# Kernel optimization log

Measured on AMD Instinct MI355X. Metric: run time of the kernel, lower is better.

The kernel has to match this reference:

```python
import jax, jax.numpy as jnp
import numpy as np

D_MODEL = 2048
H_Q = 32
H_KV = 8
D_HEAD = D_MODEL // H_Q   # 64
G = H_Q // H_KV           # 4 query heads per kv head
B, S = 2, 2048


def setup_inputs() -> dict:
    key = jax.random.key(0)
    ks = jax.random.split(key, 7)
    s = 0.02  # weight init scale
    return {
        "q": jax.random.normal(ks[0], (B, S, D_MODEL), jnp.float32),
        "k": jax.random.normal(ks[1], (B, S, D_MODEL), jnp.float32),
        "v": jax.random.normal(ks[2], (B, S, D_MODEL), jnp.float32),
        "Wq": jax.random.normal(ks[3], (D_MODEL, D_MODEL), jnp.float32) * s,
        "Wk": jax.random.normal(ks[4], (D_MODEL, H_KV * D_HEAD), jnp.float32) * s,
        "Wv": jax.random.normal(ks[5], (D_MODEL, H_KV * D_HEAD), jnp.float32) * s,
        "Wo": jax.random.normal(ks[6], (D_MODEL, D_MODEL), jnp.float32) * s,
    }


def reference(q, k, v, Wq, Wk, Wv, Wo):
    # Projections (torch Linear with bias=False: x @ W^T; here W stored as [in,out])
    b, s, _ = q.shape
    # repeat_interleave(k, G, -2) maps kv head j -> query heads j*G..j*G+G-1,
    # i.e. query head h uses kv head h // G. Reshape q heads as (H_KV, G)
    # kv-head-major instead of materializing expanded K/V.
    qh = (q @ Wq).reshape(b, s, H_KV, G, D_HEAD)
    kh = (k @ Wk).reshape(b, s, H_KV, D_HEAD)
    vh = (v @ Wv).reshape(b, s, H_KV, D_HEAD)
    scale = 1.0 / jnp.sqrt(jnp.asarray(D_HEAD, qh.dtype))
    # scores: [B, H_KV, G, Sq, Sk]
    scores = jnp.einsum('bqhgd,bkhd->bhgqk', qh, kh) * scale
    attn = jax.nn.softmax(scores, axis=-1)
    # context: [B, Sq, H_KV, G, D_HEAD]
    ctx = jnp.einsum('bhgqk,bkhd->bqhgd', attn, vh)
    out = ctx.reshape(b, s, D_MODEL) @ Wo
    return out
```

## Files before the change

### kernel.cpp

```cpp
#include <hip/hip_runtime.h>
#include <stdint.h>


typedef __attribute__((ext_vector_type(8))) short short8;
typedef __attribute__((ext_vector_type(4))) float float4v;
typedef __attribute__((ext_vector_type(4))) unsigned short ushort4v;
typedef __attribute__((ext_vector_type(4))) unsigned int uint4v;

__device__ __forceinline__ unsigned short f2bf(float f) {
  union { float f; unsigned int u; } v; v.f = f;
  unsigned int r = v.u + 0x7fffu + ((v.u >> 16) & 1u);
  return (unsigned short)(r >> 16);
}
__device__ __forceinline__ unsigned short f2bf_trunc(float f) {
  union { float f; unsigned int u; } v; v.f = f;
  return (unsigned short)(v.u >> 16);
}
__device__ __forceinline__ unsigned int fbits(float f) {
  union { float f; unsigned int u; } v; v.f = f; return v.u;
}
__device__ __forceinline__ unsigned int pack_bf16_trunc(float lo, float hi) {
  return __builtin_amdgcn_perm(fbits(hi), fbits(lo), 0x07060302u);
}

__device__ __forceinline__ void gl2lds16(const unsigned short* g, unsigned short* l) {
  __builtin_amdgcn_global_load_lds(
      (const __attribute__((address_space(1))) void*)g,
      (__attribute__((address_space(3))) void*)l, 16, 0, 0);
}

__global__ void conv3_bf16(const float* __restrict__ q, const float* __restrict__ k,
                           const float* __restrict__ v,
                           unsigned short* __restrict__ qo, unsigned short* __restrict__ ko,
                           unsigned short* __restrict__ vo, int n4) {
  const float* in;
  unsigned short* out;
  if (blockIdx.y == 0)      { in = q; out = qo; }
  else if (blockIdx.y == 1) { in = k; out = ko; }
  else                      { in = v; out = vo; }
  for (int i = blockIdx.x * blockDim.x + threadIdx.x; i < n4; i += gridDim.x * blockDim.x) {
    const float4v a = *(const float4v*)(in + (size_t)i * 4);
    *(ushort4v*)(out + (size_t)i * 4) = (ushort4v){f2bf(a.x), f2bf(a.y), f2bf(a.z), f2bf(a.w)};
  }
}

template<bool F32IN>
__global__ void transpose_bf16(const void* __restrict__ inp, unsigned short* __restrict__ out,
                               int R, int C) {
  __shared__ unsigned short t[32][33];
  const int x0 = blockIdx.x * 32, y0 = blockIdx.y * 32;
  const int tx = threadIdx.x, ty = threadIdx.y;
#pragma unroll
  for (int i = 0; i < 4; ++i) {
    const int r = y0 + ty + i * 8, c = x0 + tx;
    if (F32IN) t[ty + i * 8][tx] = f2bf(((const float*)inp)[(size_t)r * C + c]);
    else       t[ty + i * 8][tx] = ((const unsigned short*)inp)[(size_t)r * C + c];
  }
  __syncthreads();
#pragma unroll
  for (int i = 0; i < 4; ++i)
    out[(size_t)(x0 + ty + i * 8) * R + y0 + tx] = t[tx][ty + i * 8];
}

template<int TN, bool C_BF16>
__global__ __launch_bounds__(256, 2)
void gemm_bt(const unsigned short* __restrict__ A, const unsigned short* __restrict__ Bt,
             void* __restrict__ C, int N, int K, float cscale)
{
  constexpr int NT = TN / 32;
  constexpr int BI = TN / 64;
  __shared__ unsigned short As[128][32];
  __shared__ unsigned short Bs[TN][32];

  const int tid  = threadIdx.x;
  const int wave = tid >> 6;
  const int lane = tid & 63;
  const int quad = lane >> 4;
  const int l15  = lane & 15;
  const int wm   = (wave >> 1) * 64;
  const int wn   = (wave & 1) * (TN / 2);
  const int m0   = blockIdx.y * 128;
  const int n0   = blockIdx.x * TN;

  const int srow = lane >> 2;
  const int skof = (lane & 3) * 8;

  float4v acc[4][NT];
#pragma unroll
  for (int i = 0; i < 4; ++i)
#pragma unroll
    for (int j = 0; j < NT; ++j) acc[i][j] = (float4v)0.0f;

  for (int k0 = 0; k0 < K; k0 += 32) {
    __syncthreads();
#pragma unroll
    for (int i = 0; i < 2; ++i) {
      const int row = wave * 32 + i * 16 + srow;
      gl2lds16(A + (size_t)(m0 + row) * K + k0 + skof, &As[wave * 32 + i * 16][0]);
    }
#pragma unroll
    for (int i = 0; i < BI; ++i) {
      const int row = wave * (TN / 4) + i * 16 + srow;
      gl2lds16(Bt + (size_t)(n0 + row) * K + k0 + skof, &Bs[wave * (TN / 4) + i * 16][0]);
    }
    __syncthreads();

    short8 af[4], bf[NT];
#pragma unroll
    for (int mt = 0; mt < 4; ++mt)  af[mt] = *(const short8*)&As[wm + mt * 16 + l15][quad * 8];
#pragma unroll
    for (int nt = 0; nt < NT; ++nt) bf[nt] = *(const short8*)&Bs[wn + nt * 16 + l15][quad * 8];
#pragma unroll
    for (int mt = 0; mt < 4; ++mt)
#pragma unroll
      for (int nt = 0; nt < NT; ++nt)
        acc[mt][nt] = __builtin_amdgcn_mfma_f32_16x16x32_bf16(af[mt], bf[nt], acc[mt][nt], 0, 0, 0);
  }

#pragma unroll
  for (int mt = 0; mt < 4; ++mt)
#pragma unroll
    for (int nt = 0; nt < NT; ++nt) {
      const int row = m0 + wm + mt * 16 + quad * 4;
      const int col = n0 + wn + nt * 16 + l15;
#pragma unroll
      for (int r = 0; r < 4; ++r) {
        const float val = acc[mt][nt][r] * cscale;
        if (C_BF16) ((unsigned short*)C)[(size_t)(row + r) * N + col] = f2bf(val);
        else        ((float*)C)[(size_t)(row + r) * N + col] = val;
      }
    }
}

__global__ __launch_bounds__(256, 3)
void attn_flash(const unsigned short* __restrict__ Qp,
                const unsigned short* __restrict__ Kp,
                const unsigned short* __restrict__ VpT,
                unsigned short* __restrict__ Ctx)
{
  __shared__ unsigned short Ks[2][64 * 64];
  __shared__ unsigned short VTs[2][64 * 64];

  const int tid  = threadIdx.x;
  const int wave = tid >> 6;
  const int lane = tid & 63;
  const int quad = lane >> 4;
  const int l15  = lane & 15;

  const int head = blockIdx.y;
  const int b    = head >> 5;
  const int hq   = head & 31;
  const int hkv  = hq >> 2;
  const size_t qrow = (size_t)(b * 2048 + blockIdx.x * 128 + wave * 32);

  short8 qf[2][2];
#pragma unroll
  for (int mt = 0; mt < 2; ++mt)
#pragma unroll
    for (int kc = 0; kc < 2; ++kc)
      qf[mt][kc] = *(const short8*)&Qp[(qrow + mt * 16 + l15) * 2048 + hq * 64 + kc * 32 + quad * 8];

  float4v oa[2][4];
  float4v lacc[2];
#pragma unroll
  for (int mt = 0; mt < 2; ++mt) {
    lacc[mt] = (float4v)0.0f;
#pragma unroll
    for (int dt = 0; dt < 4; ++dt) oa[mt][dt] = (float4v)0.0f;
  }
  short8 ones;
#pragma unroll
  for (int i = 0; i < 8; ++i) ones[i] = (short)0x3F80;

  auto stage = [&](int j, int bu) {
#pragma unroll
    for (int i = 0; i < 2; ++i) {
      const int s  = i * 256 + wave * 64 + lane;
      const int r  = s >> 3;
      const int lc = (s & 7) ^ (r & 7);
      const int rk = ((r >> 4) & 1) * 32 + ((r >> 2) & 3) * 8 + (r >> 5) * 4 + (r & 3);
      gl2lds16(Kp + (size_t)(b * 2048 + j * 64 + rk) * 512 + hkv * 64 + lc * 8,
               &Ks[bu][i * 2048 + wave * 512]);
      gl2lds16(VpT + (size_t)(hkv * 64 + r) * 4096 + b * 2048 + j * 64 + lc * 8,
               &VTs[bu][i * 2048 + wave * 512]);
    }
  };

  stage(0, 0);
  __syncthreads();

  for (int j = 0; j < 32; ++j) {
    const int bu = j & 1;
    if (j < 31) stage(j + 1, bu ^ 1);

    short8 kf[4][2];
#pragma unroll
    for (int nt = 0; nt < 4; ++nt) {
      const int krow = nt * 16 + l15;
      kf[nt][0] = *(const short8*)&Ks[bu][krow * 64 + ((quad ^ (l15 & 7)) * 8)];
      kf[nt][1] = *(const short8*)&Ks[bu][krow * 64 + (((4 + quad) ^ (l15 & 7)) * 8)];
    }

    __builtin_amdgcn_s_setprio(1);

    unsigned int w[2][4][2];
#pragma unroll
    for (int mt = 0; mt < 2; ++mt) {
#pragma unroll
      for (int nt = 0; nt < 4; ++nt) {
        float4v sa = (float4v)0.0f;
        sa = __builtin_amdgcn_mfma_f32_16x16x32_bf16(kf[nt][0], qf[mt][0], sa, 0, 0, 0);
        sa = __builtin_amdgcn_mfma_f32_16x16x32_bf16(kf[nt][1], qf[mt][1], sa, 0, 0, 0);
        const float e0 = __builtin_amdgcn_exp2f(sa[0]);
        const float e1 = __builtin_amdgcn_exp2f(sa[1]);
        const float e2 = __builtin_amdgcn_exp2f(sa[2]);
        const float e3 = __builtin_amdgcn_exp2f(sa[3]);
        w[mt][nt][0] = pack_bf16_trunc(e0, e1);
        w[mt][nt][1] = pack_bf16_trunc(e2, e3);
      }
    }

#pragma unroll
    for (int kc = 0; kc < 2; ++kc) {
      union { uint4v u; short8 s; } p0u, p1u;
      p0u.u = (uint4v){w[0][kc][0], w[0][kc][1], w[0][kc + 2][0], w[0][kc + 2][1]};
      p1u.u = (uint4v){w[1][kc][0], w[1][kc][1], w[1][kc + 2][0], w[1][kc + 2][1]};
      const short8 pf0 = p0u.s;
      const short8 pf1 = p1u.s;
#pragma unroll
      for (int dt = 0; dt < 4; ++dt) {
        const int vrow = dt * 16 + l15;
        const short8 vf = *(const short8*)&VTs[bu][vrow * 64 + (((kc * 4 + quad) ^ (l15 & 7)) * 8)];
        oa[0][dt] = __builtin_amdgcn_mfma_f32_16x16x32_bf16(pf0, vf, oa[0][dt], 0, 0, 0);
        oa[1][dt] = __builtin_amdgcn_mfma_f32_16x16x32_bf16(pf1, vf, oa[1][dt], 0, 0, 0);
      }
      lacc[0] = __builtin_amdgcn_mfma_f32_16x16x32_bf16(pf0, ones, lacc[0], 0, 0, 0);
      lacc[1] = __builtin_amdgcn_mfma_f32_16x16x32_bf16(pf1, ones, lacc[1], 0, 0, 0);
    }

    __builtin_amdgcn_s_setprio(0);
    __syncthreads();
  }

#pragma unroll
  for (int mt = 0; mt < 2; ++mt)
#pragma unroll
    for (int r = 0; r < 4; ++r) {
      const float inv = 1.0f / lacc[mt][r];
#pragma unroll
      for (int dt = 0; dt < 4; ++dt)
        Ctx[(qrow + mt * 16 + quad * 4 + r) * 2048 + hq * 64 + dt * 16 + l15] =
            f2bf(oa[mt][dt][r] * inv);
    }
}

extern "C" void kernel_launch(void* const* d_in, const int* in_sizes, int n_in,
                              void* d_out, int out_size, void* d_ws, size_t ws_size,
                              hipStream_t stream)
{
  const float* q  = (const float*)d_in[0];
  const float* k  = (const float*)d_in[1];
  const float* v  = (const float*)d_in[2];
  const float* Wq = (const float*)d_in[3];
  const float* Wk = (const float*)d_in[4];
  const float* Wv = (const float*)d_in[5];
  const float* Wo = (const float*)d_in[6];
  float* out = (float*)d_out;

  unsigned short* ws  = (unsigned short*)d_ws;
  unsigned short* qb  = ws;
  unsigned short* kb  = qb  + (size_t)8388608;
  unsigned short* vb  = kb  + (size_t)8388608;
  unsigned short* WT  = vb  + (size_t)8388608;
  unsigned short* Qp  = WT  + (size_t)4194304;
  unsigned short* Kp  = Qp  + (size_t)8388608;
  unsigned short* VpT = Kp  + (size_t)2097152;
  unsigned short* Ctx = qb;

  const dim3 blk(256);
  const dim3 tblk(32, 8);
  const float SM_SCALE = 0.125f * 1.44269504089f;

  conv3_bf16<<<dim3(512, 3), blk, 0, stream>>>(q, k, v, qb, kb, vb, 8388608 / 4);

  transpose_bf16<true><<<dim3(64, 64), tblk, 0, stream>>>(Wq, WT, 2048, 2048);
  gemm_bt<128, true><<<dim3(16, 32), blk, 0, stream>>>(qb, WT, Qp, 2048, 2048, SM_SCALE);

  transpose_bf16<true><<<dim3(16, 64), tblk, 0, stream>>>(Wk, WT, 2048, 512);
  gemm_bt<64, true><<<dim3(8, 32), blk, 0, stream>>>(kb, WT, Kp, 512, 2048, 1.0f);

  transpose_bf16<true><<<dim3(16, 64), tblk, 0, stream>>>(Wv, WT, 2048, 512);
  gemm_bt<64, true><<<dim3(64, 4), blk, 0, stream>>>(WT, vb, VpT, 4096, 2048, 1.0f);

  attn_flash<<<dim3(16, 64), blk, 0, stream>>>(Qp, Kp, VpT, Ctx);

  transpose_bf16<true><<<dim3(64, 64), tblk, 0, stream>>>(Wo, WT, 2048, 2048);
  gemm_bt<128, false><<<dim3(16, 32), blk, 0, stream>>>(Ctx, WT, out, 2048, 2048, 1.0f);
}
```

Measured before the change: 413.7 us.

## Merge prep kernels and K/V projections into fewer launches, raise attention occupancy

Folds the three input fp32-to-bf16 conversions and the Wq/Wk/Wv transposes into one multi-role prep launch. The K and V projection GEMMs become a single launch that dispatches on block id, and the Wo transpose moves ahead of attention. The goal is to cut kernel launch count and let small, underfilled kernels share the GPU. It also raises attn_flash launch bounds from 3 to 4 blocks per CU, which may constrain registers. The Q GEMM now writes into a workspace region that temporarily holds the transposed K/V weights, so it relies on stream ordering.

```diff
diff --git a/kernel.cpp b/kernel.cpp
--- a/kernel.cpp
+++ b/kernel.cpp
@@ -12,10 +12,6 @@
   unsigned int r = v.u + 0x7fffu + ((v.u >> 16) & 1u);
   return (unsigned short)(r >> 16);
 }
-__device__ __forceinline__ unsigned short f2bf_trunc(float f) {
-  union { float f; unsigned int u; } v; v.f = f;
-  return (unsigned short)(v.u >> 16);
-}
 __device__ __forceinline__ unsigned int fbits(float f) {
   union { float f; unsigned int u; } v; v.f = f; return v.u;
 }
@@ -29,23 +25,47 @@
       (__attribute__((address_space(3))) void*)l, 16, 0, 0);
 }
 
-__global__ void conv3_bf16(const float* __restrict__ q, const float* __restrict__ k,
-                           const float* __restrict__ v,
-                           unsigned short* __restrict__ qo, unsigned short* __restrict__ ko,
-                           unsigned short* __restrict__ vo, int n4) {
-  const float* in;
-  unsigned short* out;
-  if (blockIdx.y == 0)      { in = q; out = qo; }
-  else if (blockIdx.y == 1) { in = k; out = ko; }
-  else                      { in = v; out = vo; }
-  for (int i = blockIdx.x * blockDim.x + threadIdx.x; i < n4; i += gridDim.x * blockDim.x) {
-    const float4v a = *(const float4v*)(in + (size_t)i * 4);
-    *(ushort4v*)(out + (size_t)i * 4) = (ushort4v){f2bf(a.x), f2bf(a.y), f2bf(a.z), f2bf(a.w)};
-  }
-}
-
-template<bool F32IN>
-__global__ void transpose_bf16(const void* __restrict__ inp, unsigned short* __restrict__ out,
+__global__ void prep(const float* __restrict__ q, const float* __restrict__ k,
+                     const float* __restrict__ v,
+                     const float* __restrict__ Wq, const float* __restrict__ Wk,
+                     const float* __restrict__ Wv,
+                     unsigned short* __restrict__ qb, unsigned short* __restrict__ kb,
+                     unsigned short* __restrict__ vb,
+                     unsigned short* __restrict__ WTq, unsigned short* __restrict__ WTk,
+                     unsigned short* __restrict__ WTv)
+{
+  __shared__ unsigned short t[32][33];
+  const int z = blockIdx.z;
+  if (z >= 3) {
+    const float* in  = (z == 3) ? q : (z == 4) ? k : v;
+    unsigned short* out = (z == 3) ? qb : (z == 4) ? kb : vb;
+    const int tid = threadIdx.y * 32 + threadIdx.x;
+    const int bid = blockIdx.y * 64 + blockIdx.x;
+    for (int i = bid * 256 + tid; i < 2097152; i += 4096 * 256) {
+      const float4v a = *(const float4v*)(in + (size_t)i * 4);
+      *(ushort4v*)(out + (size_t)i * 4) = (ushort4v){f2bf(a.x), f2bf(a.y), f2bf(a.z), f2bf(a.w)};
+    }
+    return;
+  }
+  const float* in; unsigned short* out; int R, C;
+  if (z == 0)      { in = Wq; out = WTq; R = 2048; C = 2048; }
+  else if (z == 1) { in = Wk; out = WTk; R = 2048; C = 512; }
+  else             { in = Wv; out = WTv; R = 2048; C = 512; }
+  const int x0 = blockIdx.x * 32, y0 = blockIdx.y * 32;
+  if (x0 >= C) return;
+  const int tx = threadIdx.x, ty = threadIdx.y;
+#pragma unroll
+  for (int i = 0; i < 4; ++i) {
+    const int r = y0 + ty + i * 8, c = x0 + tx;
+    t[ty + i * 8][tx] = f2bf(in[(size_t)r * C + c]);
+  }
+  __syncthreads();
+#pragma unroll
+  for (int i = 0; i < 4; ++i)
+    out[(size_t)(x0 + ty + i * 8) * R + y0 + tx] = t[tx][ty + i * 8];
+}
+
+__global__ void transpose_bf16(const float* __restrict__ inp, unsigned short* __restrict__ out,
                                int R, int C) {
   __shared__ unsigned short t[32][33];
   const int x0 = blockIdx.x * 32, y0 = blockIdx.y * 32;
@@ -53,8 +73,7 @@
 #pragma unroll
   for (int i = 0; i < 4; ++i) {
     const int r = y0 + ty + i * 8, c = x0 + tx;
-    if (F32IN) t[ty + i * 8][tx] = f2bf(((const float*)inp)[(size_t)r * C + c]);
-    else       t[ty + i * 8][tx] = ((const unsigned short*)inp)[(size_t)r * C + c];
+    t[ty + i * 8][tx] = f2bf(inp[(size_t)r * C + c]);
   }
   __syncthreads();
 #pragma unroll
@@ -63,9 +82,10 @@
 }
 
 template<int TN, bool C_BF16>
-__global__ __launch_bounds__(256, 2)
-void gemm_bt(const unsigned short* __restrict__ A, const unsigned short* __restrict__ Bt,
-             void* __restrict__ C, int N, int K, float cscale)
+__device__ void gemm_body(const unsigned short* __restrict__ A,
+                          const unsigned short* __restrict__ Bt,
+                          void* __restrict__ C, int N, int K, float cscale,
+                          int bx, int by)
 {
   constexpr int NT = TN / 32;
   constexpr int BI = TN / 64;
@@ -79,8 +99,8 @@
   const int l15  = lane & 15;
   const int wm   = (wave >> 1) * 64;
   const int wn   = (wave & 1) * (TN / 2);
-  const int m0   = blockIdx.y * 128;
-  const int n0   = blockIdx.x * TN;
+  const int m0   = by * 128;
+  const int n0   = bx * TN;
 
   const int srow = lane >> 2;
   const int skof = (lane & 3) * 8;
@@ -132,7 +152,26 @@
     }
 }
 
-__global__ __launch_bounds__(256, 3)
+template<int TN, bool C_BF16>
+__global__ __launch_bounds__(256, 2)
+void gemm_bt(const unsigned short* __restrict__ A, const unsigned short* __restrict__ Bt,
+             void* __restrict__ C, int N, int K, float cscale)
+{
+  gemm_body<TN, C_BF16>(A, Bt, C, N, K, cscale, blockIdx.x, blockIdx.y);
+}
+
+__global__ __launch_bounds__(256, 2)
+void gemm_kv(const unsigned short* __restrict__ kb, const unsigned short* __restrict__ WTk,
+             unsigned short* __restrict__ Kp,
+             const unsigned short* __restrict__ WTv, const unsigned short* __restrict__ vb,
+             unsigned short* __restrict__ VpT)
+{
+  const int id = blockIdx.x;
+  if (id < 256) gemm_body<64, true>(kb, WTk, Kp, 512, 2048, 1.0f, id & 7, id >> 3);
+  else          gemm_body<64, true>(WTv, vb, VpT, 4096, 2048, 1.0f, (id - 256) & 63, (id - 256) >> 6);
+}
+
+__global__ __launch_bounds__(256, 4)
 void attn_flash(const unsigned short* __restrict__ Qp,
                 const unsigned short* __restrict__ Kp,
                 const unsigned short* __restrict__ VpT,
@@ -276,24 +315,23 @@
   unsigned short* Kp  = Qp  + (size_t)8388608;
   unsigned short* VpT = Kp  + (size_t)2097152;
   unsigned short* Ctx = qb;
+  unsigned short* WTk = Qp;
+  unsigned short* WTv = Qp + (size_t)1048576;
 
   const dim3 blk(256);
   const dim3 tblk(32, 8);
   const float SM_SCALE = 0.125f * 1.44269504089f;
 
-  conv3_bf16<<<dim3(512, 3), blk, 0, stream>>>(q, k, v, qb, kb, vb, 8388608 / 4);
-
-  transpose_bf16<true><<<dim3(64, 64), tblk, 0, stream>>>(Wq, WT, 2048, 2048);
+  prep<<<dim3(64, 64, 6), tblk, 0, stream>>>(q, k, v, Wq, Wk, Wv,
+                                             qb, kb, vb, WT, WTk, WTv);
+
+  gemm_kv<<<dim3(512), blk, 0, stream>>>(kb, WTk, Kp, WTv, vb, VpT);
+
   gemm_bt<128, true><<<dim3(16, 32), blk, 0, stream>>>(qb, WT, Qp, 2048, 2048, SM_SCALE);
 
-  transpose_bf16<true><<<dim3(16, 64), tblk, 0, stream>>>(Wk, WT, 2048, 512);
-  gemm_bt<64, true><<<dim3(8, 32), blk, 0, stream>>>(kb, WT, Kp, 512, 2048, 1.0f);
-
-  transpose_bf16<true><<<dim3(16, 64), tblk, 0, stream>>>(Wv, WT, 2048, 512);
-  gemm_bt<64, true><<<dim3(64, 4), blk, 0, stream>>>(WT, vb, VpT, 4096, 2048, 1.0f);
+  transpose_bf16<<<dim3(64, 64), tblk, 0, stream>>>(Wo, WT, 2048, 2048);
 
   attn_flash<<<dim3(16, 64), blk, 0, stream>>>(Qp, Kp, VpT, Ctx);
 
-  transpose_bf16<true><<<dim3(64, 64), tblk, 0, stream>>>(Wo, WT, 2048, 2048);
   gemm_bt<128, false><<<dim3(16, 32), blk, 0, stream>>>(Ctx, WT, out, 2048, 2048, 1.0f);
 }
```

After: 382.7 us. 7.5% less time.
